# Kernel tuning notes

Hardware: AMD Instinct MI355X
Metric: run time of the kernel (lower is better)

The kernel has to match this reference:

```python
import jax, jax.numpy as jnp
import numpy as np

D_MODEL = 1024
N_HEAD = 16
D_HEAD = D_MODEL // N_HEAD


def setup_inputs() -> dict:
    key = jax.random.key(0)
    k_x, k_wqkv, k_bqkv, k_wp, k_bp = jax.random.split(key, 5)
    B, T = 2, 2048
    bound = 1.0 / np.sqrt(D_MODEL)
    return {
        "x": jax.random.normal(k_x, (B, T, D_MODEL), dtype=jnp.float32),
        "w_qkv": jax.random.uniform(k_wqkv, (D_MODEL, 3 * D_MODEL), jnp.float32, -bound, bound),
        "b_qkv": jax.random.uniform(k_bqkv, (3 * D_MODEL,), jnp.float32, -bound, bound),
        "w_proj": jax.random.uniform(k_wp, (D_MODEL, D_MODEL), jnp.float32, -bound, bound),
        "b_proj": jax.random.uniform(k_bp, (D_MODEL,), jnp.float32, -bound, bound),
    }


def reference(x, w_qkv, b_qkv, w_proj, b_proj):
    B, T, C = x.shape
    qkv = x @ w_qkv + b_qkv                       # [B,T,3C]
    qkv = qkv.reshape(B, T, 3, N_HEAD, D_HEAD)
    qkv = jnp.transpose(qkv, (2, 0, 3, 1, 4))      # [3,B,H,T,dh]
    q, k, v = qkv[0], qkv[1], qkv[2]
    scale = np.sqrt(D_HEAD).astype(np.float32)
    attn = jnp.einsum("bhqd,bhkd->bhqk", q, k) / scale  # [B,H,T,T]
    causal = jnp.tril(jnp.ones((T, T), dtype=bool))
    attn = jnp.where(causal, attn, -jnp.inf)
    attn = jax.nn.softmax(attn, axis=-1)
    out = jnp.einsum("bhqk,bhkd->bhqd", attn, v)   # [B,H,T,dh]
    out = jnp.transpose(out, (0, 2, 1, 3)).reshape(B, T, C)
    return out @ w_proj + b_proj
```

## Files before the change

### kernel.cpp

```cpp
#include <hip/hip_runtime.h>
#include <hip/hip_bf16.h>
#include <math.h>

constexpr int Bb   = 2;
constexpr int T    = 2048;
constexpr int C    = 1024;
constexpr int H    = 16;
constexpr int M    = Bb * T;
constexpr int NQKV = 3 * C;

typedef __attribute__((ext_vector_type(8))) short bf16x8;
typedef __attribute__((ext_vector_type(4))) float f32x4;

__device__ inline short f2bf(float f) {
    __hip_bfloat16 h = __float2bfloat16(f);
    return *reinterpret_cast<short*>(&h);
}

#if __has_builtin(__builtin_amdgcn_exp2f)
#define EXP2(x) __builtin_amdgcn_exp2f(x)
#else
#define EXP2(x) exp2f(x)
#endif

#define GLOBAL_AS __attribute__((address_space(1)))
#define LDS_AS    __attribute__((address_space(3)))

__device__ __forceinline__ void gload_lds16(const short* g, short* s) {
    __builtin_amdgcn_global_load_lds((const GLOBAL_AS void*)g, (LDS_AS void*)s, 16, 0, 0);
}

__global__ __launch_bounds__(256)
void prep_all(const float* __restrict__ x, short* __restrict__ xb,
              const float* __restrict__ w_qkv, short* __restrict__ wqkvt,
              const float* __restrict__ w_proj, short* __restrict__ wprojt)
{
    __shared__ float tile[32][33];
    const int blk = blockIdx.x;
    const int tid = threadIdx.x;

    if (blk < 4096) {
        const int i = blk * 1024 + tid * 4;
        const float4 v = *(const float4*)(x + i);
        short4 s;
        s.x = f2bf(v.x); s.y = f2bf(v.y); s.z = f2bf(v.z); s.w = f2bf(v.w);
        *(short4*)(xb + i) = s;
        return;
    }

    const bool isqkv = (blk < 7168);
    const int bidx = isqkv ? (blk - 4096) : (blk - 7168);
    const int nblk = isqkv ? 96 : 32;
    const int N    = isqkv ? NQKV : C;
    const float* W = isqkv ? w_qkv : w_proj;
    short* Wt      = isqkv ? wqkvt : wprojt;

    const int n0 = (bidx % nblk) * 32, k0 = (bidx / nblk) * 32;
    const int tx = tid & 31, ty = tid >> 5;
#pragma unroll
    for (int i = 0; i < 32; i += 8)
        tile[ty + i][tx] = W[(size_t)(k0 + ty + i) * N + n0 + tx];
    __syncthreads();
#pragma unroll
    for (int i = 0; i < 32; i += 8)
        Wt[(size_t)(n0 + ty + i) * C + k0 + tx] = f2bf(tile[tx][ty + i]);
}

__global__ __launch_bounds__(256)
void gemm_mfma(const short* __restrict__ A, const short* __restrict__ Bt,
               const float* __restrict__ bias, short* __restrict__ outp,
               int Ndim, int Kdim)
{
    __shared__ __align__(16) short As[128 * 32];
    __shared__ __align__(16) short Bs[128 * 32];

    const int tid = threadIdx.x;
    const int w   = tid >> 6;
    const int l   = tid & 63;
    const int lk  = l & 15;
    const int lq  = l >> 4;
    const int m0  = blockIdx.y * 128, n0 = blockIdx.x * 128;
    const int mw  = (w >> 1) * 64, nw = (w & 1) * 64;

    const int srow = w * 16 + (l >> 2);
    const int scol = (l & 3) * 8;
    short* asdst0 = &As[w * 512];
    short* asdst1 = &As[2048 + w * 512];
    short* bsdst0 = &Bs[w * 512];
    short* bsdst1 = &Bs[2048 + w * 512];

    f32x4 acc[4][4];
#pragma unroll
    for (int i = 0; i < 4; ++i)
#pragma unroll
        for (int j = 0; j < 4; ++j) acc[i][j] = (f32x4){0.f, 0.f, 0.f, 0.f};

    for (int k0 = 0; k0 < Kdim; k0 += 32) {
        __syncthreads();
        gload_lds16(A  + (size_t)(m0 + srow)      * Kdim + k0 + scol, asdst0);
        gload_lds16(A  + (size_t)(m0 + 64 + srow) * Kdim + k0 + scol, asdst1);
        gload_lds16(Bt + (size_t)(n0 + srow)      * Kdim + k0 + scol, bsdst0);
        gload_lds16(Bt + (size_t)(n0 + 64 + srow) * Kdim + k0 + scol, bsdst1);
        __syncthreads();

        bf16x8 af[4], bfr[4];
#pragma unroll
        for (int mt = 0; mt < 4; ++mt)
            af[mt] = *(const bf16x8*)&As[(mw + mt * 16 + lk) * 32 + lq * 8];
#pragma unroll
        for (int nt = 0; nt < 4; ++nt)
            bfr[nt] = *(const bf16x8*)&Bs[(nw + nt * 16 + lk) * 32 + lq * 8];
#pragma unroll
        for (int mt = 0; mt < 4; ++mt)
#pragma unroll
            for (int nt = 0; nt < 4; ++nt)
                acc[mt][nt] = __builtin_amdgcn_mfma_f32_16x16x32_bf16(bfr[nt], af[mt], acc[mt][nt], 0, 0, 0);
    }

    float4 bv[4];
#pragma unroll
    for (int nt = 0; nt < 4; ++nt)
        bv[nt] = *(const float4*)(bias + n0 + nw + nt * 16 + lq * 4);
#pragma unroll
    for (int mt = 0; mt < 4; ++mt) {
        short* rowp = outp + (size_t)(m0 + mw + mt * 16 + lk) * Ndim + n0 + nw + lq * 4;
#pragma unroll
        for (int nt = 0; nt < 4; ++nt) {
            short4 pk;
            pk.x = f2bf(acc[mt][nt][0] + bv[nt].x);
            pk.y = f2bf(acc[mt][nt][1] + bv[nt].y);
            pk.z = f2bf(acc[mt][nt][2] + bv[nt].z);
            pk.w = f2bf(acc[mt][nt][3] + bv[nt].w);
            *(short4*)(rowp + nt * 16) = pk;
        }
    }
}

__global__ __launch_bounds__(256)
void gemm_mfma_proj(const short* __restrict__ A, const short* __restrict__ Bt,
                    const float* __restrict__ bias, float* __restrict__ outp,
                    int Ndim, int Kdim)
{
    __shared__ __align__(16) short As[64 * 32];
    __shared__ __align__(16) short Bs[128 * 32];

    const int tid = threadIdx.x;
    const int w   = tid >> 6;
    const int l   = tid & 63;
    const int lk  = l & 15;
    const int lq  = l >> 4;
    const int m0  = blockIdx.y * 64, n0 = blockIdx.x * 128;
    const int mw  = (w & 1) * 32, nw = (w >> 1) * 64;

    const int srow = w * 16 + (l >> 2);
    const int scol = (l & 3) * 8;
    short* asdst  = &As[w * 512];
    short* bsdst0 = &Bs[w * 512];
    short* bsdst1 = &Bs[2048 + w * 512];

    f32x4 acc[2][4];
#pragma unroll
    for (int i = 0; i < 2; ++i)
#pragma unroll
        for (int j = 0; j < 4; ++j) acc[i][j] = (f32x4){0.f, 0.f, 0.f, 0.f};

    for (int k0 = 0; k0 < Kdim; k0 += 32) {
        __syncthreads();
        gload_lds16(A  + (size_t)(m0 + srow)      * Kdim + k0 + scol, asdst);
        gload_lds16(Bt + (size_t)(n0 + srow)      * Kdim + k0 + scol, bsdst0);
        gload_lds16(Bt + (size_t)(n0 + 64 + srow) * Kdim + k0 + scol, bsdst1);
        __syncthreads();

        bf16x8 af[2], bfr[4];
#pragma unroll
        for (int mt = 0; mt < 2; ++mt)
            af[mt] = *(const bf16x8*)&As[(mw + mt * 16 + lk) * 32 + lq * 8];
#pragma unroll
        for (int nt = 0; nt < 4; ++nt)
            bfr[nt] = *(const bf16x8*)&Bs[(nw + nt * 16 + lk) * 32 + lq * 8];
#pragma unroll
        for (int mt = 0; mt < 2; ++mt)
#pragma unroll
            for (int nt = 0; nt < 4; ++nt)
                acc[mt][nt] = __builtin_amdgcn_mfma_f32_16x16x32_bf16(bfr[nt], af[mt], acc[mt][nt], 0, 0, 0);
    }

    float4 bv[4];
#pragma unroll
    for (int nt = 0; nt < 4; ++nt)
        bv[nt] = *(const float4*)(bias + n0 + nw + nt * 16 + lq * 4);
#pragma unroll
    for (int mt = 0; mt < 2; ++mt) {
        float* rowp = outp + (size_t)(m0 + mw + mt * 16 + lk) * Ndim + n0 + nw + lq * 4;
#pragma unroll
        for (int nt = 0; nt < 4; ++nt) {
            float4 v;
            v.x = acc[mt][nt][0] + bv[nt].x;
            v.y = acc[mt][nt][1] + bv[nt].y;
            v.z = acc[mt][nt][2] + bv[nt].z;
            v.w = acc[mt][nt][3] + bv[nt].w;
            *(float4*)(rowp + nt * 16) = v;
        }
    }
}

constexpr int LDV = 136;
constexpr float SC = 0.18033688f;

__global__ __launch_bounds__(256, 4)
void attn_mfma(const short* __restrict__ qkv, short* __restrict__ att)
{
    __shared__ __align__(16) short Ks[128 * 64];
    __shared__ __align__(16) short Vt[64 * LDV];

    const int idx = blockIdx.x;
    const int xcd = idx & 7;
    const int j   = idx >> 3;
    const int bh  = xcd * 4 + (j & 3);
    const int s   = j >> 2;
    const int qt  = (s < 8)  ? (31 - s)
                  : (s < 16) ? (s - 8)
                  : (s < 24) ? (39 - s)
                  :            (s - 16);
    const int b   = bh >> 4;
    const int h   = bh & 15;
    const int qbase = qt * 64;

    const int tid = threadIdx.x;
    const int w   = tid >> 6;
    const int l   = tid & 63;
    const int lk  = l & 15;
    const int lq  = l >> 4;

    const short* base = qkv + (size_t)b * T * 3072 + h * 64;

    const int q_abs = qbase + w * 16 + lk;
    const short* qp = base + (size_t)q_abs * 3072 + lq * 8;
    const bf16x8 qf0 = *(const bf16x8*)qp;
    const bf16x8 qf1 = *(const bf16x8*)(qp + 32);

    f32x4 acc_o[4];
#pragma unroll
    for (int dt = 0; dt < 4; ++dt) acc_o[dt] = (f32x4){0.f, 0.f, 0.f, 0.f};
    float m_run = -INFINITY;
    float l_run = 0.f;

    const int krow   = l >> 3;
    const int kcolsw = 8 * ((l & 7) ^ (l >> 3));
    const int swz    = lk & 7;

    const int kg   = tid & 31;
    const int vd0  = (tid >> 5) * 8;
    const int pcol = ((kg & 24) | ((kg & 3) << 1) | ((kg >> 2) & 1)) * 4;

    const int nkt = (qbase + 64 + 127) >> 7;
#pragma unroll 1
    for (int it = 0; it < nkt; ++it) {
        const int j0 = it * 128;
        __syncthreads();
#pragma unroll
        for (int rr = 0; rr < 4; ++rr) {
            const int g = w * 32 + rr * 8;
            gload_lds16(base + 1024 + (size_t)(j0 + g + krow) * 3072 + kcolsw, &Ks[g * 64]);
        }
        {
            const short* vp = base + 2048 + (size_t)(j0 + kg * 4) * 3072 + vd0;
            bf16x8 vv[4];
#pragma unroll
            for (int kk = 0; kk < 4; ++kk)
                vv[kk] = *(const bf16x8*)(vp + (size_t)kk * 3072);
#pragma unroll
            for (int d = 0; d < 8; ++d) {
                short4 pk;
                pk.x = vv[0][d]; pk.y = vv[1][d]; pk.z = vv[2][d]; pk.w = vv[3][d];
                *(short4*)&Vt[(vd0 + d) * LDV + pcol] = pk;
            }
        }
        __syncthreads();

        f32x4 s4[8];
#pragma unroll
        for (int kt = 0; kt < 8; ++kt) {
            const int row = kt * 16 + lk;
            const bf16x8 kf0 = *(const bf16x8*)&Ks[row * 64 + 8 * (lq ^ swz)];
            const bf16x8 kf1 = *(const bf16x8*)&Ks[row * 64 + 8 * ((lq + 4) ^ swz)];
            f32x4 a = (f32x4){0.f, 0.f, 0.f, 0.f};
            a = __builtin_amdgcn_mfma_f32_16x16x32_bf16(kf0, qf0, a, 0, 0, 0);
            a = __builtin_amdgcn_mfma_f32_16x16x32_bf16(kf1, qf1, a, 0, 0, 0);
            s4[kt] = a;
        }

        if (it == nkt - 1) {
#pragma unroll
            for (int kt = 0; kt < 8; ++kt)
#pragma unroll
                for (int r = 0; r < 4; ++r)
                    if (j0 + kt * 16 + lq * 4 + r > q_abs) s4[kt][r] = -1e30f;
        }

        float mx = s4[0][0];
#pragma unroll
        for (int kt = 0; kt < 8; ++kt)
#pragma unroll
            for (int r = 0; r < 4; ++r) mx = fmaxf(mx, s4[kt][r]);
        mx = fmaxf(mx, __shfl_xor(mx, 16));
        mx = fmaxf(mx, __shfl_xor(mx, 32));
        const float mn   = fmaxf(m_run, mx);
        const float corr = EXP2((m_run - mn) * SC);
        m_run = mn;
        const float nmc = -mn * SC;
#pragma unroll
        for (int kt = 0; kt < 8; ++kt)
#pragma unroll
            for (int r = 0; r < 4; ++r)
                s4[kt][r] = EXP2(fmaf(s4[kt][r], SC, nmc));
        float ps = 0.f;
#pragma unroll
        for (int kt = 0; kt < 8; ++kt)
            ps += ((s4[kt][0] + s4[kt][1]) + (s4[kt][2] + s4[kt][3]));
        ps += __shfl_xor(ps, 16);
        ps += __shfl_xor(ps, 32);
        l_run = l_run * corr + ps;

        unsigned int d0[8], d1[8];
#pragma unroll
        for (int kt = 0; kt < 8; ++kt) {
            d0[kt] = (unsigned int)(unsigned short)f2bf(s4[kt][0])
                   | ((unsigned int)(unsigned short)f2bf(s4[kt][1]) << 16);
            d1[kt] = (unsigned int)(unsigned short)f2bf(s4[kt][2])
                   | ((unsigned int)(unsigned short)f2bf(s4[kt][3]) << 16);
        }

#pragma unroll
        for (int dt = 0; dt < 4; ++dt)
#pragma unroll
            for (int r = 0; r < 4; ++r) acc_o[dt][r] *= corr;

#pragma unroll
        for (int kc = 0; kc < 4; ++kc) {
            union { unsigned int u[4]; bf16x8 v; } up;
            up.u[0] = d0[kc * 2];
            up.u[1] = d1[kc * 2];
            up.u[2] = d0[kc * 2 + 1];
            up.u[3] = d1[kc * 2 + 1];
            const bf16x8 pf = up.v;
#pragma unroll
            for (int dt = 0; dt < 4; ++dt) {
                const bf16x8 vf = *(const bf16x8*)&Vt[(dt * 16 + lk) * LDV + kc * 32 + lq * 8];
                acc_o[dt] = __builtin_amdgcn_mfma_f32_16x16x32_bf16(vf, pf, acc_o[dt], 0, 0, 0);
            }
        }
    }

    const float inv = 1.f / l_run;
    short* op = att + ((size_t)(b * T + q_abs)) * 1024 + h * 64;
#pragma unroll
    for (int dt = 0; dt < 4; ++dt) {
        short4 pk;
        pk.x = f2bf(acc_o[dt][0] * inv);
        pk.y = f2bf(acc_o[dt][1] * inv);
        pk.z = f2bf(acc_o[dt][2] * inv);
        pk.w = f2bf(acc_o[dt][3] * inv);
        *(short4*)(op + dt * 16 + lq * 4) = pk;
    }
}

extern "C" void kernel_launch(void* const* d_in, const int* in_sizes, int n_in,
                              void* d_out, int out_size, void* d_ws, size_t ws_size,
                              hipStream_t stream)
{
    const float* x      = (const float*)d_in[0];
    const float* w_qkv  = (const float*)d_in[1];
    const float* b_qkv  = (const float*)d_in[2];
    const float* w_proj = (const float*)d_in[3];
    const float* b_proj = (const float*)d_in[4];
    float* out = (float*)d_out;

    short* xb     = (short*)d_ws;
    short* wqkvt  = xb     + (size_t)M * C;
    short* wprojt = wqkvt  + (size_t)NQKV * C;
    short* qkvb   = wprojt + (size_t)C * C;
    short* attb   = qkvb   + (size_t)M * NQKV;

    prep_all<<<8192, 256, 0, stream>>>(x, xb, w_qkv, wqkvt, w_proj, wprojt);
    gemm_mfma<<<dim3(NQKV / 128, M / 128), 256, 0, stream>>>(xb, wqkvt, b_qkv, qkvb, NQKV, C);
    attn_mfma<<<1024, 256, 0, stream>>>(qkvb, attb);
    gemm_mfma_proj<<<dim3(C / 128, M / 64), 256, 0, stream>>>(attb, wprojt, b_proj, out, C, C);
}
```

Baseline: 189.7 us.

## Double-buffer LDS tiles in GEMM kernels and swizzle workgroup order

Both the QKV and projection GEMMs now use two LDS buffers, so the global-to-LDS loads for the next K step are issued before the MFMAs on the current step and one barrier per iteration is removed. Workgroup IDs are also remapped with an interleave of eight, which changes which tiles run concurrently and so may change L2 reuse. This doubles LDS use per block and can lower occupancy. The swizzle assumes the workgroup count is divisible by eight.

```diff
diff --git a/kernel.cpp b/kernel.cpp
--- a/kernel.cpp
+++ b/kernel.cpp
@@ -71,23 +71,37 @@
                const float* __restrict__ bias, short* __restrict__ outp,
                int Ndim, int Kdim)
 {
-    __shared__ __align__(16) short As[128 * 32];
-    __shared__ __align__(16) short Bs[128 * 32];
+    __shared__ __align__(16) short As[2 * 128 * 32];
+    __shared__ __align__(16) short Bs[2 * 128 * 32];
 
     const int tid = threadIdx.x;
     const int w   = tid >> 6;
     const int l   = tid & 63;
     const int lk  = l & 15;
     const int lq  = l >> 4;
-    const int m0  = blockIdx.y * 128, n0 = blockIdx.x * 128;
+
+    const int gx  = gridDim.x;
+    const int nwg = gx * gridDim.y;
+    const int cpx = nwg >> 3;
+    const int bid = blockIdx.y * gx + blockIdx.x;
+    const int swz = (bid & 7) * cpx + (bid >> 3);
+    const int m0  = (swz / gx) * 128;
+    const int n0  = (swz % gx) * 128;
+
     const int mw  = (w >> 1) * 64, nw = (w & 1) * 64;
 
     const int srow = w * 16 + (l >> 2);
     const int scol = (l & 3) * 8;
-    short* asdst0 = &As[w * 512];
-    short* asdst1 = &As[2048 + w * 512];
-    short* bsdst0 = &Bs[w * 512];
-    short* bsdst1 = &Bs[2048 + w * 512];
+
+    const short* agp0 = A  + (size_t)(m0 + srow)      * Kdim + scol;
+    const short* agp1 = A  + (size_t)(m0 + 64 + srow) * Kdim + scol;
+    const short* bgp0 = Bt + (size_t)(n0 + srow)      * Kdim + scol;
+    const short* bgp1 = Bt + (size_t)(n0 + 64 + srow) * Kdim + scol;
+
+    short* ad0 = &As[w * 512];
+    short* ad1 = &As[2048 + w * 512];
+    short* bd0 = &Bs[w * 512];
+    short* bd1 = &Bs[2048 + w * 512];
 
     f32x4 acc[4][4];
 #pragma unroll
@@ -95,26 +109,40 @@
 #pragma unroll
         for (int j = 0; j < 4; ++j) acc[i][j] = (f32x4){0.f, 0.f, 0.f, 0.f};
 
+    gload_lds16(agp0, ad0);
+    gload_lds16(agp1, ad1);
+    gload_lds16(bgp0, bd0);
+    gload_lds16(bgp1, bd1);
+    __syncthreads();
+
+    int cur = 0;
     for (int k0 = 0; k0 < Kdim; k0 += 32) {
-        __syncthreads();
-        gload_lds16(A  + (size_t)(m0 + srow)      * Kdim + k0 + scol, asdst0);
-        gload_lds16(A  + (size_t)(m0 + 64 + srow) * Kdim + k0 + scol, asdst1);
-        gload_lds16(Bt + (size_t)(n0 + srow)      * Kdim + k0 + scol, bsdst0);
-        gload_lds16(Bt + (size_t)(n0 + 64 + srow) * Kdim + k0 + scol, bsdst1);
-        __syncthreads();
+        const int coff = cur ? 4096 : 0;
 
         bf16x8 af[4], bfr[4];
 #pragma unroll
         for (int mt = 0; mt < 4; ++mt)
-            af[mt] = *(const bf16x8*)&As[(mw + mt * 16 + lk) * 32 + lq * 8];
+            af[mt] = *(const bf16x8*)&As[coff + (mw + mt * 16 + lk) * 32 + lq * 8];
 #pragma unroll
         for (int nt = 0; nt < 4; ++nt)
-            bfr[nt] = *(const bf16x8*)&Bs[(nw + nt * 16 + lk) * 32 + lq * 8];
+            bfr[nt] = *(const bf16x8*)&Bs[coff + (nw + nt * 16 + lk) * 32 + lq * 8];
+
+        if (k0 + 32 < Kdim) {
+            const int noff = cur ? 0 : 4096;
+            gload_lds16(agp0 + k0 + 32, ad0 + noff);
+            gload_lds16(agp1 + k0 + 32, ad1 + noff);
+            gload_lds16(bgp0 + k0 + 32, bd0 + noff);
+            gload_lds16(bgp1 + k0 + 32, bd1 + noff);
+        }
+
 #pragma unroll
         for (int mt = 0; mt < 4; ++mt)
 #pragma unroll
             for (int nt = 0; nt < 4; ++nt)
                 acc[mt][nt] = __builtin_amdgcn_mfma_f32_16x16x32_bf16(bfr[nt], af[mt], acc[mt][nt], 0, 0, 0);
+
+        __syncthreads();
+        cur ^= 1;
     }
 
     float4 bv[4];
@@ -141,22 +169,35 @@
                     const float* __restrict__ bias, float* __restrict__ outp,
                     int Ndim, int Kdim)
 {
-    __shared__ __align__(16) short As[64 * 32];
-    __shared__ __align__(16) short Bs[128 * 32];
+    __shared__ __align__(16) short As[2 * 64 * 32];
+    __shared__ __align__(16) short Bs[2 * 128 * 32];
 
     const int tid = threadIdx.x;
     const int w   = tid >> 6;
     const int l   = tid & 63;
     const int lk  = l & 15;
     const int lq  = l >> 4;
-    const int m0  = blockIdx.y * 64, n0 = blockIdx.x * 128;
+
+    const int gx  = gridDim.x;
+    const int nwg = gx * gridDim.y;
+    const int cpx = nwg >> 3;
+    const int bid = blockIdx.y * gx + blockIdx.x;
+    const int swz = (bid & 7) * cpx + (bid >> 3);
+    const int m0  = (swz / gx) * 64;
+    const int n0  = (swz % gx) * 128;
+
     const int mw  = (w & 1) * 32, nw = (w >> 1) * 64;
 
     const int srow = w * 16 + (l >> 2);
     const int scol = (l & 3) * 8;
-    short* asdst  = &As[w * 512];
-    short* bsdst0 = &Bs[w * 512];
-    short* bsdst1 = &Bs[2048 + w * 512];
+
+    const short* agp  = A  + (size_t)(m0 + srow)      * Kdim + scol;
+    const short* bgp0 = Bt + (size_t)(n0 + srow)      * Kdim + scol;
+    const short* bgp1 = Bt + (size_t)(n0 + 64 + srow) * Kdim + scol;
+
+    short* ad  = &As[w * 512];
+    short* bd0 = &Bs[w * 512];
+    short* bd1 = &Bs[2048 + w * 512];
 
     f32x4 acc[2][4];
 #pragma unroll
@@ -164,25 +205,40 @@
 #pragma unroll
         for (int j = 0; j < 4; ++j) acc[i][j] = (f32x4){0.f, 0.f, 0.f, 0.f};
 
+    gload_lds16(agp,  ad);
+    gload_lds16(bgp0, bd0);
+    gload_lds16(bgp1, bd1);
+    __syncthreads();
+
+    int cur = 0;
     for (int k0 = 0; k0 < Kdim; k0 += 32) {
-        __syncthreads();
-        gload_lds16(A  + (size_t)(m0 + srow)      * Kdim + k0 + scol, asdst);
-        gload_lds16(Bt + (size_t)(n0 + srow)      * Kdim + k0 + scol, bsdst0);
-        gload_lds16(Bt + (size_t)(n0 + 64 + srow) * Kdim + k0 + scol, bsdst1);
-        __syncthreads();
+        const int coffA = cur ? 2048 : 0;
+        const int coffB = cur ? 4096 : 0;
 
         bf16x8 af[2], bfr[4];
 #pragma unroll
         for (int mt = 0; mt < 2; ++mt)
-            af[mt] = *(const bf16x8*)&As[(mw + mt * 16 + lk) * 32 + lq * 8];
+            af[mt] = *(const bf16x8*)&As[coffA + (mw + mt * 16 + lk) * 32 + lq * 8];
 #pragma unroll
         for (int nt = 0; nt < 4; ++nt)
-            bfr[nt] = *(const bf16x8*)&Bs[(nw + nt * 16 + lk) * 32 + lq * 8];
+            bfr[nt] = *(const bf16x8*)&Bs[coffB + (nw + nt * 16 + lk) * 32 + lq * 8];
+
+        if (k0 + 32 < Kdim) {
+            const int noffA = cur ? 0 : 2048;
+            const int noffB = cur ? 0 : 4096;
+            gload_lds16(agp  + k0 + 32, ad  + noffA);
+            gload_lds16(bgp0 + k0 + 32, bd0 + noffB);
+            gload_lds16(bgp1 + k0 + 32, bd1 + noffB);
+        }
+
 #pragma unroll
         for (int mt = 0; mt < 2; ++mt)
 #pragma unroll
             for (int nt = 0; nt < 4; ++nt)
                 acc[mt][nt] = __builtin_amdgcn_mfma_f32_16x16x32_bf16(bfr[nt], af[mt], acc[mt][nt], 0, 0, 0);
+
+        __syncthreads();
+        cur ^= 1;
     }
 
     float4 bv[4];
```

Measured after the change: 179.8 us. -5.2%, faster.
